# Kernel optimization log

Hardware: AMD Instinct MI355X
Metric: run time of the kernel (lower is better)

## Reference

```python
import jax, jax.numpy as jnp
import numpy as np

ATOMS_PER_RES = 24  # hard-coded in .view(B, N_l, -1, 24)
NEG_SLOPE = 0.01    # nn.LeakyReLU default


def setup_inputs() -> dict:
    key = jax.random.key(0)
    ks = jax.random.split(key, 10)
    B, N_l, N_p, H, G = 16, 64, 512, 128, 10
    pos_l = jax.random.normal(ks[0], (B, N_l, 3), jnp.float32) * 5.0
    pos_p = jax.random.normal(ks[1], (B, N_p, ATOMS_PER_RES, 3), jnp.float32) * 5.0
    Interact = jax.random.normal(ks[2], (B, N_l, N_p, H), jnp.float32)
    Interact_mask = jax.random.randint(ks[3], (B, N_l, N_p), 0, 2) > 0
    W_pi = jax.random.normal(ks[4], (H, G), jnp.float32) * 0.05
    b_pi = jnp.zeros((G,), jnp.float32)
    W_sigma = jax.random.normal(ks[5], (H, G), jnp.float32) * 0.05
    b_sigma = jnp.zeros((G,), jnp.float32)
    W_mu = jax.random.normal(ks[6], (H, G), jnp.float32) * 0.05
    b_mu = jnp.zeros((G,), jnp.float32)
    return {
        "pos_l": pos_l, "pos_p": pos_p, "Interact": Interact,
        "Interact_mask": Interact_mask,
        "W_pi": W_pi, "b_pi": b_pi,
        "W_sigma": W_sigma, "b_sigma": b_sigma,
        "W_mu": W_mu, "b_mu": b_mu,
    }


def _min_dist(pos_l, pos_p):
    # pos_l: [B, N_l, 3]; pos_p: [B, N_p, 24, 3]
    B, N_l, _ = pos_l.shape
    Y = pos_p.reshape(B, -1, 3)  # [B, N_p*24, 3]
    d2 = (jnp.sum(pos_l * pos_l, axis=-1)[..., None]
          + jnp.sum(Y * Y, axis=-1)[:, None, :]
          - 2.0 * jnp.einsum('bic,bjc->bij', pos_l, Y))  # [B, N_l, N_p*24]
    dist = jnp.nan_to_num(jnp.sqrt(d2), nan=10000.0)
    # min over the 24 atoms of each residue -> [B, N_l, N_p]
    return dist.reshape(B, N_l, -1, ATOMS_PER_RES).min(axis=-1)


def reference(pos_l, pos_p, Interact, Interact_mask,
              W_pi, b_pi, W_sigma, b_sigma, W_mu, b_mu):
    leaky = lambda x: jax.nn.leaky_relu(x, NEG_SLOPE)
    dist = _min_dist(pos_l, pos_p)                       # [B, N_l, N_p]
    # original gathers dist[Interact_mask]; keep static shape, zero-fill masked-out
    dist_masked = jnp.where(Interact_mask, dist, 0.0)
    pi = jax.nn.softmax(Interact @ W_pi + b_pi, axis=-1)          # [B,N_l,N_p,G]
    sigma = jnp.clip(leaky(Interact @ W_sigma + b_sigma) + 1.1, 1e-6, None)
    mu = leaky(Interact @ W_mu + b_mu) + 1.0
    return pi, sigma, mu, dist_masked, Interact_mask
```

## Files before the change

### kernel.cpp

```cpp
#include <hip/hip_runtime.h>
#include <cmath>

#define NB 16
#define NL 64
#define NP 512
#define NH 128
#define NG 10
#define ROWS (NB * NL * NP)

#define OFF_PI    ((size_t)0)
#define OFF_SIGMA ((size_t)5242880)
#define OFF_MU    ((size_t)10485760)
#define OFF_DIST  ((size_t)15728640)
#define OFF_MASK  ((size_t)16252928)

__global__ __launch_bounds__(256) void k_dist(
    const float* __restrict__ pos_l,
    const float* __restrict__ pos_p,
    const int*   __restrict__ mask,
    float* __restrict__ dist_out,
    float* __restrict__ mask_out)
{
    int idx = blockIdx.x * 256 + threadIdx.x;
    int p  = idx & (NP - 1);
    int bl = idx >> 9;
    int b  = bl >> 6;

    const float* xl = pos_l + bl * 3;
    float x0 = xl[0], x1 = xl[1], x2 = xl[2];
    float xs = x0 * x0 + x1 * x1 + x2 * x2;

    const float4* yp = (const float4*)(pos_p + ((size_t)(b * NP + p)) * 72);

    float m = 1e30f;
    #pragma unroll
    for (int q = 0; q < 6; ++q) {
        float4 v0 = yp[q * 3 + 0];
        float4 v1 = yp[q * 3 + 1];
        float4 v2 = yp[q * 3 + 2];
        float c[12] = {v0.x, v0.y, v0.z, v0.w,
                       v1.x, v1.y, v1.z, v1.w,
                       v2.x, v2.y, v2.z, v2.w};
        #pragma unroll
        for (int a = 0; a < 4; ++a) {
            float yx = c[a * 3 + 0], yy = c[a * 3 + 1], yz = c[a * 3 + 2];
            float d2 = xs + (yx * yx + yy * yy + yz * yz)
                          - 2.0f * (x0 * yx + x1 * yy + x2 * yz);
            float s = (d2 >= 0.0f) ? sqrtf(d2) : 10000.0f;
            m = fminf(m, s);
        }
    }

    int mk = mask[idx];
    dist_out[idx] = mk ? m : 0.0f;
    mask_out[idx] = mk ? 1.0f : 0.0f;
}

__global__ __launch_bounds__(256) void k_gemv(
    const float* __restrict__ X,
    const float* __restrict__ Wpi, const float* __restrict__ bpi,
    const float* __restrict__ Wsg, const float* __restrict__ bsg,
    const float* __restrict__ Wmu, const float* __restrict__ bmu,
    float* __restrict__ out_pi,
    float* __restrict__ out_sg,
    float* __restrict__ out_mu)
{
    __shared__ float lw[NH * 32];
    __shared__ float lb[32];
    int tid = threadIdx.x;

    for (int i = tid; i < NH * 32; i += 256) {
        int k = i >> 5, g = i & 31;
        float v = 0.0f;
        if      (g < 10) v = Wpi[k * NG + g];
        else if (g < 20) v = Wsg[k * NG + (g - 10)];
        else if (g < 30) v = Wmu[k * NG + (g - 20)];
        lw[i] = v;
    }
    if (tid < 32) {
        float v = 0.0f;
        if      (tid < 10) v = bpi[tid];
        else if (tid < 20) v = bsg[tid - 10];
        else if (tid < 30) v = bmu[tid - 20];
        lb[tid] = v;
    }
    __syncthreads();

    int row = blockIdx.x * 256 + tid;
    const float4* xr  = (const float4*)(X + (size_t)row * NH);
    const float4* lw4 = (const float4*)lw;

    float4 acc[8];
    #pragma unroll
    for (int g4 = 0; g4 < 8; ++g4) acc[g4] = ((const float4*)lb)[g4];

    #pragma unroll 4
    for (int k4 = 0; k4 < 32; ++k4) {
        float4 h = xr[k4];
        float hk[4] = {h.x, h.y, h.z, h.w};
        #pragma unroll
        for (int kk = 0; kk < 4; ++kk) {
            const float4* wrow = lw4 + (size_t)(k4 * 4 + kk) * 8;
            float hv = hk[kk];
            #pragma unroll
            for (int g4 = 0; g4 < 8; ++g4) {
                float4 w = wrow[g4];
                acc[g4].x = fmaf(hv, w.x, acc[g4].x);
                acc[g4].y = fmaf(hv, w.y, acc[g4].y);
                acc[g4].z = fmaf(hv, w.z, acc[g4].z);
                acc[g4].w = fmaf(hv, w.w, acc[g4].w);
            }
        }
    }

    float a[32];
    #pragma unroll
    for (int g4 = 0; g4 < 8; ++g4) {
        a[g4 * 4 + 0] = acc[g4].x; a[g4 * 4 + 1] = acc[g4].y;
        a[g4 * 4 + 2] = acc[g4].z; a[g4 * 4 + 3] = acc[g4].w;
    }

    size_t ro = (size_t)row * NG;

    float mx = a[0];
    #pragma unroll
    for (int g = 1; g < NG; ++g) mx = fmaxf(mx, a[g]);
    float e[NG], s = 0.0f;
    #pragma unroll
    for (int g = 0; g < NG; ++g) { e[g] = __expf(a[g] - mx); s += e[g]; }
    float inv = 1.0f / s;
    #pragma unroll
    for (int g = 0; g < NG; ++g) out_pi[ro + g] = e[g] * inv;

    #pragma unroll
    for (int g = 0; g < NG; ++g) {
        float x = a[10 + g];
        float v = (x >= 0.0f ? x : 0.01f * x) + 1.1f;
        out_sg[ro + g] = fmaxf(v, 1e-6f);
    }

    #pragma unroll
    for (int g = 0; g < NG; ++g) {
        float x = a[20 + g];
        out_mu[ro + g] = (x >= 0.0f ? x : 0.01f * x) + 1.0f;
    }
}

extern "C" void kernel_launch(void* const* d_in, const int* in_sizes, int n_in,
                              void* d_out, int out_size, void* d_ws, size_t ws_size,
                              hipStream_t stream) {
    const float* pos_l    = (const float*)d_in[0];
    const float* pos_p    = (const float*)d_in[1];
    const float* Interact = (const float*)d_in[2];
    const int*   mask     = (const int*)  d_in[3];
    const float* Wpi      = (const float*)d_in[4];
    const float* bpi      = (const float*)d_in[5];
    const float* Wsg      = (const float*)d_in[6];
    const float* bsg      = (const float*)d_in[7];
    const float* Wmu      = (const float*)d_in[8];
    const float* bmu      = (const float*)d_in[9];

    float* out      = (float*)d_out;
    float* out_pi   = out + OFF_PI;
    float* out_sg   = out + OFF_SIGMA;
    float* out_mu   = out + OFF_MU;
    float* out_dist = out + OFF_DIST;
    float* out_mask = out + OFF_MASK;

    hipLaunchKernelGGL(k_dist, dim3(ROWS / 256), dim3(256), 0, stream,
                       pos_l, pos_p, mask, out_dist, out_mask);
    hipLaunchKernelGGL(k_gemv, dim3(ROWS / 256), dim3(256), 0, stream,
                       Interact, Wpi, bpi, Wsg, bsg, Wmu, bmu,
                       out_pi, out_sg, out_mu);
}
```

Before: 448.9 us.

## Register-block gemv over four rows per thread to reuse LDS weights

Each thread now computes four rows instead of one, so every weight float4 read from shared memory feeds four rows of FMAs. The grid shrinks fourfold and launch bounds request two blocks per CU. This targets LDS bandwidth as the bottleneck of the projection, at the cost of 128 accumulator registers, lower occupancy and fewer blocks to spread across CUs.

Result: slower. 634.5 us (+41.3%).

```diff
diff --git a/kernel.cpp b/kernel.cpp
--- a/kernel.cpp
+++ b/kernel.cpp
@@ -56,7 +56,7 @@
     mask_out[idx] = mk ? 1.0f : 0.0f;
 }
 
-__global__ __launch_bounds__(256) void k_gemv(
+__global__ __launch_bounds__(256, 2) void k_gemv(
     const float* __restrict__ X,
     const float* __restrict__ Wpi, const float* __restrict__ bpi,
     const float* __restrict__ Wsg, const float* __restrict__ bsg,
@@ -86,63 +86,87 @@
     }
     __syncthreads();
 
-    int row = blockIdx.x * 256 + tid;
-    const float4* xr  = (const float4*)(X + (size_t)row * NH);
     const float4* lw4 = (const float4*)lw;
+    int base = blockIdx.x * 1024 + tid;
 
-    float4 acc[8];
+    const float4* xr[4];
     #pragma unroll
-    for (int g4 = 0; g4 < 8; ++g4) acc[g4] = ((const float4*)lb)[g4];
+    for (int r = 0; r < 4; ++r)
+        xr[r] = (const float4*)(X + (size_t)(base + r * 256) * NH);
 
-    #pragma unroll 4
-    for (int k4 = 0; k4 < 32; ++k4) {
-        float4 h = xr[k4];
-        float hk[4] = {h.x, h.y, h.z, h.w};
+    float4 acc[4][8];
+    {
+        float4 bias[8];
         #pragma unroll
-        for (int kk = 0; kk < 4; ++kk) {
-            const float4* wrow = lw4 + (size_t)(k4 * 4 + kk) * 8;
-            float hv = hk[kk];
+        for (int g4 = 0; g4 < 8; ++g4) bias[g4] = ((const float4*)lb)[g4];
+        #pragma unroll
+        for (int r = 0; r < 4; ++r)
+            #pragma unroll
+            for (int g4 = 0; g4 < 8; ++g4) acc[r][g4] = bias[g4];
+    }
+
+    for (int c = 0; c < 16; ++c) {
+        float4 xa[4], xb[4];
+        #pragma unroll
+        for (int r = 0; r < 4; ++r) {
+            xa[r] = xr[r][c * 2 + 0];
+            xb[r] = xr[r][c * 2 + 1];
+        }
+        #pragma unroll
+        for (int kk = 0; kk < 8; ++kk) {
+            float hv[4];
+            #pragma unroll
+            for (int r = 0; r < 4; ++r) {
+                const float* xs4 = (kk < 4) ? (const float*)&xa[r] : (const float*)&xb[r];
+                hv[r] = xs4[kk & 3];
+            }
+            const float4* wrow = lw4 + (size_t)(c * 8 + kk) * 8;
             #pragma unroll
             for (int g4 = 0; g4 < 8; ++g4) {
                 float4 w = wrow[g4];
-                acc[g4].x = fmaf(hv, w.x, acc[g4].x);
-                acc[g4].y = fmaf(hv, w.y, acc[g4].y);
-                acc[g4].z = fmaf(hv, w.z, acc[g4].z);
-                acc[g4].w = fmaf(hv, w.w, acc[g4].w);
+                #pragma unroll
+                for (int r = 0; r < 4; ++r) {
+                    acc[r][g4].x = fmaf(hv[r], w.x, acc[r][g4].x);
+                    acc[r][g4].y = fmaf(hv[r], w.y, acc[r][g4].y);
+                    acc[r][g4].z = fmaf(hv[r], w.z, acc[r][g4].z);
+                    acc[r][g4].w = fmaf(hv[r], w.w, acc[r][g4].w);
+                }
             }
         }
     }
 
-    float a[32];
     #pragma unroll
-    for (int g4 = 0; g4 < 8; ++g4) {
-        a[g4 * 4 + 0] = acc[g4].x; a[g4 * 4 + 1] = acc[g4].y;
-        a[g4 * 4 + 2] = acc[g4].z; a[g4 * 4 + 3] = acc[g4].w;
-    }
+    for (int r = 0; r < 4; ++r) {
+        float a[32];
+        #pragma unroll
+        for (int g4 = 0; g4 < 8; ++g4) {
+            a[g4 * 4 + 0] = acc[r][g4].x; a[g4 * 4 + 1] = acc[r][g4].y;
+            a[g4 * 4 + 2] = acc[r][g4].z; a[g4 * 4 + 3] = acc[r][g4].w;
+        }
+        size_t ro = (size_t)(base + r * 256) * NG;
 
-    size_t ro = (size_t)row * NG;
+        float mx = a[0];
+        #pragma unroll
+        for (int g = 1; g < NG; ++g) mx = fmaxf(mx, a[g]);
+        float e[NG], s = 0.0f;
+        #pragma unroll
+        for (int g = 0; g < NG; ++g) { e[g] = __expf(a[g] - mx); s += e[g]; }
+        float inv = 1.0f / s;
+        #pragma unroll
+        for (int g = 0; g < NG; ++g) out_pi[ro + g] = e[g] * inv;
 
-    float mx = a[0];
-    #pragma unroll
-    for (int g = 1; g < NG; ++g) mx = fmaxf(mx, a[g]);
-    float e[NG], s = 0.0f;
-    #pragma unroll
-    for (int g = 0; g < NG; ++g) { e[g] = __expf(a[g] - mx); s += e[g]; }
-    float inv = 1.0f / s;
-    #pragma unroll
-    for (int g = 0; g < NG; ++g) out_pi[ro + g] = e[g] * inv;
+        #pragma unroll
+        for (int g = 0; g < NG; ++g) {
+            float x = a[10 + g];
+            float v = (x >= 0.0f ? x : 0.01f * x) + 1.1f;
+            out_sg[ro + g] = fmaxf(v, 1e-6f);
+        }
 
-    #pragma unroll
-    for (int g = 0; g < NG; ++g) {
-        float x = a[10 + g];
-        float v = (x >= 0.0f ? x : 0.01f * x) + 1.1f;
-        out_sg[ro + g] = fmaxf(v, 1e-6f);
-    }
-
-    #pragma unroll
-    for (int g = 0; g < NG; ++g) {
-        float x = a[20 + g];
-        out_mu[ro + g] = (x >= 0.0f ? x : 0.01f * x) + 1.0f;
+        #pragma unroll
+        for (int g = 0; g < NG; ++g) {
+            float x = a[20 + g];
+            out_mu[ro + g] = (x >= 0.0f ? x : 0.01f * x) + 1.0f;
+        }
     }
 }
 
@@ -169,7 +193,7 @@
 
     hipLaunchKernelGGL(k_dist, dim3(ROWS / 256), dim3(256), 0, stream,
                        pos_l, pos_p, mask, out_dist, out_mask);
-    hipLaunchKernelGGL(k_gemv, dim3(ROWS / 256), dim3(256), 0, stream,
+    hipLaunchKernelGGL(k_gemv, dim3(ROWS / 1024), dim3(256), 0, stream,
                        Interact, Wpi, bpi, Wsg, bsg, Wmu, bmu,
                        out_pi, out_sg, out_mu);
 }
```
